# Kernel optimization log

Measured on AMD Instinct MI355X. Metric: run time of the kernel, lower is better.

Reference implementation:

```python
import jax, jax.numpy as jnp
import numpy as np

# graph structure constants (uniform graphs => simple coloring / masks all-true)
G, NV, EPG, LEPG = 128, 32, 64, 256          # graphs, nodes/graph, g-edges/graph, lg-edges/graph
NG, NLG, ELG, K = G * NV, G * EPG, G * LEPG, EPG  # K = n_colors = lg-nodes per graph
H, HF, T, L, NC, FIN, FE, NB = 32, 128, 8, 4, 12, 16, 16, 4  # hidden, hidden_final, towers, layers, classes, node feats, edge feats, basis

_FLOATS = ('x_g','edge_attr_g','x_lg','edge_attr_lg','W_enc','b_enc','W_msg','b_msg','W_init','b_init','np_l1_w','np_l1_b','np_l2_w','np_l2_b','np_lin_w','np_lin_b','fe_l1_w','fe_l1_b','fe_l2_w','fe_l2_b','fe_lin_w','fe_lin_b','gd_w','gd_b','ga_w','ga_b','ld_w','ld_b','la_w','la_b','u1_w','u1_b','u2_w','u2_b','u3_w','u3_b','en_w','en_b','li_w','li_b','lj_w','lj_b','bn_g','bn_b','ac_w','ac_b','fl_w','fl_b')

def _lin(x, w, b):
    return x @ w + b

def _glin(x, w, b):
    # grouped (tower) linear: w [T, c, c], block-diagonal over channel groups
    t, ci, co = w.shape
    y = jnp.einsum('...tc,tcd->...td', x.reshape(x.shape[:-1] + (t, ci)), w)
    return y.reshape(x.shape[:-1] + (t * co,)) + b

def setup_inputs():
    rng = np.random.default_rng(0)
    off_n = np.arange(G)[:, None] * NV
    ei_g = np.stack([(rng.integers(0, NV, (G, EPG)) + off_n).ravel(),
                     (rng.integers(0, NV, (G, EPG)) + off_n).ravel()])
    off_e = np.arange(G)[:, None] * EPG
    ei_lg = np.stack([(rng.integers(0, EPG, (G, LEPG)) + off_e).ravel(),
                      (rng.integers(0, EPG, (G, LEPG)) + off_e).ravel()])
    keys = iter(jax.random.split(jax.random.key(0), 64))
    def nrm(shape, fan):
        return (jax.random.normal(next(keys), shape, dtype=jnp.float32) / np.float32(np.sqrt(fan)))
    z = lambda *s: jnp.zeros(s, jnp.float32)
    inp = {
        'x_g': nrm((NG, FIN), 1.0),
        'edge_attr_g': nrm((NLG, FE), 1.0),
        'x_lg': nrm((NLG, NB), 1.0),
        'edge_attr_lg': nrm((ELG, NB), 1.0),
        'W_enc': nrm((FIN, H), FIN), 'b_enc': z(H),
        'W_msg': nrm((2 * H + FE + NB, HF), 2 * H + FE + NB), 'b_msg': z(HF),
        'W_init': nrm((HF + 1, H), HF + 1), 'b_init': z(H),
        'np_l1_w': nrm((HF + 1, HF), HF + 1), 'np_l1_b': z(HF),
        'np_l2_w': nrm((HF + 1, HF), HF + 1), 'np_l2_b': z(HF),
        'np_lin_w': nrm((HF, HF), HF), 'np_lin_b': z(HF),
        'fe_l1_w': nrm((H, HF), H), 'fe_l1_b': z(HF),
        'fe_l2_w': nrm((H, HF), H), 'fe_l2_b': z(HF),
        'fe_lin_w': nrm((HF, HF), HF), 'fe_lin_b': z(HF),
        'gd_w': nrm((NB, NB), NB), 'gd_b': z(NB),
        'ga_w': nrm((NB, NB), NB), 'ga_b': z(NB),
        'ld_w': nrm((L, NB, H), NB), 'ld_b': z(L, H),
        'la_w': nrm((L, NB, H), NB), 'la_b': z(L, H),
        'u1_w': nrm((L, T, H // T, H // T), H // T), 'u1_b': z(L, H),
        'u2_w': nrm((L, T, H // T, H // T), H // T), 'u2_b': z(L, H),
        'u3_w': nrm((L, T, H // T, H // T), H // T), 'u3_b': z(L, H),
        'en_w': nrm((L, H, H), H), 'en_b': z(L, H),
        'li_w': nrm((L, T, H // T, H // T), H // T), 'li_b': z(L, H),
        'lj_w': nrm((L, T, H // T, H // T), H // T), 'lj_b': z(L, H),
        'bn_g': jnp.ones((L, H), jnp.float32), 'bn_b': z(L, H),
        'ac_w': nrm((HF, HF), HF), 'ac_b': z(HF),
        'fl_w': nrm((HF, NC), HF), 'fl_b': z(NC),
        'edge_index_g': jnp.asarray(ei_g, dtype=jnp.int32),
        'edge_index_lg': jnp.asarray(ei_lg, dtype=jnp.int32),
        'batch_g': jnp.asarray(np.repeat(np.arange(G), NV), dtype=jnp.int32),
    }
    return inp

def _forward(fl, edge_index_g, edge_index_lg, batch_g):
    p = dict(zip(_FLOATS, fl))
    h = _lin(p['x_g'], p['W_enc'], p['b_enc'])                                 # [NG, H]
    s, d = edge_index_g[0], edge_index_g[1]
    hm = _lin(jnp.concatenate([h[s], h[d], p['edge_attr_g'], p['x_lg']], -1),
              p['W_msg'], p['b_msg'])                                          # [NLG, HF]
    batch_lg = batch_g[s]                                                      # graph id per lg node
    coloring = jnp.arange(NLG, dtype=jnp.int32) - batch_lg * EPG               # local color in [0, K)
    onehot = (coloring[:, None] == jnp.arange(K)).astype(hm.dtype)             # [NLG, K]
    # map_x_to_u: one-hot identity channel + features on own color row
    u = jnp.concatenate([onehot[:, :, None], onehot[:, :, None] * hm[:, None, :]], 2)  # [NLG, K, HF+1]
    edge_glob = _lin(p['edge_attr_lg'], p['ga_w'], p['ga_b'])                  # [ELG, NB]
    dist_glob = _lin(p['x_lg'], p['gd_w'], p['gd_b'])                          # [NLG, NB]
    ls, ld = edge_index_lg[0], edge_index_lg[1]
    indeg = jax.ops.segment_sum(jnp.ones((ELG,), hm.dtype), ld, num_segments=NLG)
    avg_e = (jax.ops.segment_sum(indeg, batch_lg, num_segments=G) / EPG)[batch_lg]  # avg edges/graph per node
    idx = jnp.arange(NLG)
    nb = jnp.asarray(EPG, hm.dtype)                                            # lg nodes per graph

    def extract(u, w1, b1, w2, b2, lw, lb):
        # GraphExtractor: UtoGlobal (mean-over-colors pool + diagonal pool) + residual relu lin
        mean = jax.ops.segment_sum(u.sum(1) / nb, batch_lg, num_segments=G) / nb
        diag = jax.ops.segment_sum(u[idx, coloring], batch_lg, num_segments=G) / nb
        out = _lin(mean, w1, b1) + _lin(diag, w2, b2)
        return out + jax.nn.relu(_lin(out, lw, lb))

    out = extract(u, p['np_l1_w'], p['np_l1_b'], p['np_l2_w'], p['np_l2_b'], p['np_lin_w'], p['np_lin_b'])
    u = _lin(u, p['W_init'], p['b_init'])                                      # [NLG, K, H]
    for i in range(L):
        if i > 0:  # batch norm (training-mode stats over nodes x colors)
            m = u.mean((0, 1)); v = u.var((0, 1))
            u = (u - m) * jax.lax.rsqrt(v + 1e-5) * p['bn_g'][i] + p['bn_b'][i]
        dist_loc = _lin(dist_glob, p['ld_w'][i], p['ld_b'][i])                 # [NLG, H]
        edge_loc = _lin(edge_glob, p['la_w'][i], p['la_b'][i])                 # [ELG, H]
        # SMPLayer: UtoU message net (entrywise + color-mean + diagonal terms, towered)
        um = (_glin(u, p['u1_w'][i], p['u1_b'][i])
              + _glin(u.sum(1) / nb, p['u2_w'][i], p['u2_b'][i])[:, None, :]
              + _glin(u[idx, coloring], p['u3_w'][i], p['u3_b'][i])[:, None, :])
        um = um * dist_loc[:, None, :]                                         # distance-basis filter
        ui = _glin(um, p['li_w'][i], p['li_b'][i])
        uj = _glin(um, p['lj_w'][i], p['lj_b'][i])
        ef = _lin(edge_loc, p['en_w'][i], p['en_b'][i])[:, None, :]
        msg = um[ls] + jax.nn.relu(ui[ld] + uj[ls] + ef)                       # [ELG, K, H]
        u = jax.ops.segment_sum(msg, ld, num_segments=NLG) / avg_e[:, None, None] + u
        out = out + extract(u, p['fe_l1_w'], p['fe_l1_b'], p['fe_l2_w'], p['fe_l2_b'], p['fe_lin_w'], p['fe_lin_b']) / L
    out = jax.nn.relu(_lin(out, p['ac_w'], p['ac_b'])) + out
    return _lin(out, p['fl_w'], p['fl_b'])                                     # [G, NC]

def reference(x_g, edge_attr_g, x_lg, edge_attr_lg, W_enc, b_enc, W_msg, b_msg, W_init, b_init, np_l1_w, np_l1_b, np_l2_w, np_l2_b, np_lin_w, np_lin_b, fe_l1_w, fe_l1_b, fe_l2_w, fe_l2_b, fe_lin_w, fe_lin_b, gd_w, gd_b, ga_w, ga_b, ld_w, ld_b, la_w, la_b, u1_w, u1_b, u2_w, u2_b, u3_w, u3_b, en_w, en_b, li_w, li_b, lj_w, lj_b, bn_g, bn_b, ac_w, ac_b, fl_w, fl_b, edge_index_g, edge_index_lg, batch_g):
    args = dict(locals())
    fl = tuple(args[n] for n in _FLOATS)
    return _forward(fl, edge_index_g, edge_index_lg, batch_g)
```

## Files before the change

kernel.cpp:

```cpp
#include <hip/hip_runtime.h>

#define G_    128
#define NV_   32
#define EPG_  64
#define LEPG_ 256
#define NG_   (G_*NV_)
#define NLG_  (G_*EPG_)
#define ELG_  (G_*LEPG_)
#define K_    64
#define H_    32
#define HF_   128
#define L_    4
#define NC_   12
#define FIN_  16
#define FE_   16
#define NB_   4
#define TILE_ (K_*H_)

__global__ void k_init(float* sc, float* sh, float* bn_acc) {
    int t = threadIdx.x;
    if (t < 32) { sc[t] = 1.0f; sh[t] = 0.0f; }
    if (t < 256) bn_acc[t] = 0.0f;
}

__global__ void k_enc(const float* __restrict__ xg, const float* __restrict__ W,
                      const float* __restrict__ b, float* __restrict__ h) {
    int gid = blockIdx.x * 256 + threadIdx.x;
    int n = gid >> 5, ch = gid & 31;
    float s = b[ch];
#pragma unroll
    for (int f = 0; f < FIN_; ++f) s += xg[n*FIN_ + f] * W[f*H_ + ch];
    h[gid] = s;
}

__global__ __launch_bounds__(128) void k_msg(
    const float* __restrict__ h, const float* __restrict__ eag,
    const float* __restrict__ xlg, const int* __restrict__ sidx,
    const int* __restrict__ didx, const float* __restrict__ W,
    const float* __restrict__ b, float* __restrict__ hm) {
    __shared__ float in[84];
    int i = blockIdx.x, t = threadIdx.x;
    int s = sidx[i], d = didx[i];
    if (t < 32)       in[t] = h[s*H_ + t];
    else if (t < 64)  in[t] = h[d*H_ + (t-32)];
    else if (t < 80)  in[t] = eag[i*FE_ + (t-64)];
    else if (t < 84)  in[t] = xlg[i*NB_ + (t-80)];
    __syncthreads();
    float o = b[t];
    for (int k = 0; k < 84; ++k) o += in[k] * W[k*HF_ + t];
    hm[i*HF_ + t] = o;
}

__global__ void k_glob(const float* __restrict__ ealg, const float* __restrict__ gaw,
                       const float* __restrict__ gab, const float* __restrict__ xlg,
                       const float* __restrict__ gdw, const float* __restrict__ gdb,
                       float* __restrict__ eglob, float* __restrict__ dglob) {
    int gid = blockIdx.x * 256 + threadIdx.x;
    if (gid < ELG_*4) {
        int e = gid >> 2, k = gid & 3;
        float s = gab[k];
#pragma unroll
        for (int j = 0; j < 4; ++j) s += ealg[e*4+j] * gaw[j*4+k];
        eglob[gid] = s;
    }
    int gid2 = gid - ELG_*4;
    if (gid2 >= 0 && gid2 < NLG_*4) {
        int n = gid2 >> 2, k = gid2 & 3;
        float s = gdb[k];
#pragma unroll
        for (int j = 0; j < 4; ++j) s += xlg[n*4+j] * gdw[j*4+k];
        dglob[gid2] = s;
    }
}

__global__ __launch_bounds__(128) void k_out0(
    const float* __restrict__ hm, const float* __restrict__ l1w,
    const float* __restrict__ l1b, const float* __restrict__ l2w,
    const float* __restrict__ l2b, const float* __restrict__ lnw,
    const float* __restrict__ lnb, float* __restrict__ out_acc) {
    __shared__ float mh[128], o1[128];
    int g = blockIdx.x, t = threadIdx.x;
    float s = 0.f;
    for (int k = 0; k < 64; ++k) s += hm[(g*64+k)*HF_ + t];
    mh[t] = s * (1.f/64.f);
    __syncthreads();
    float o = l1b[t] + l2b[t] + (l1w[t]*(1.f/64.f) + l2w[t]);
    for (int k = 0; k < 128; ++k)
        o += mh[k] * (l1w[(1+k)*HF_ + t]*(1.f/64.f) + l2w[(1+k)*HF_ + t]);
    o1[t] = o;
    __syncthreads();
    float r = lnb[t];
    for (int k = 0; k < 128; ++k) r += o1[k] * lnw[k*HF_ + t];
    out_acc[g*HF_ + t] = o + (r > 0.f ? r : 0.f);
}

__global__ __launch_bounds__(256) void k_u0(
    const float* __restrict__ hm, const float* __restrict__ Wi,
    const float* __restrict__ bi, float* __restrict__ u0,
    float* __restrict__ nst) {
    __shared__ float rv[32];
    int n = blockIdx.x, t = threadIdx.x, cn = n & 63;
    if (t < 32) {
        float s = Wi[t];
        for (int f = 0; f < HF_; ++f) s += hm[n*HF_ + f] * Wi[(1+f)*H_ + t];
        rv[t] = s;
    }
    __syncthreads();
#pragma unroll
    for (int k = 0; k < 8; ++k) {
        int idx = t + k*256;
        int ch = idx >> 6, c = idx & 63;
        u0[(size_t)n*TILE_ + idx] = bi[ch] + (c == cn ? rv[ch] : 0.f);
    }
    if (t < 32) {
        nst[n*96 + t]      = 64.f*bi[t] + rv[t];
        nst[n*96 + 32 + t] = bi[t] + rv[t];
    }
}

__global__ void k_dl(const float* __restrict__ dgl, const float* __restrict__ ldw,
                     const float* __restrict__ ldb, float* __restrict__ dlb) {
    int gid = blockIdx.x * 256 + threadIdx.x;
    int n = gid >> 5, ch = gid & 31;
    float s = ldb[ch];
#pragma unroll
    for (int j = 0; j < 4; ++j) s += dgl[n*4+j] * ldw[j*32 + ch];
    dlb[gid] = s;
}

__global__ __launch_bounds__(128) void k_ef(
    const float* __restrict__ egl, const float* __restrict__ law,
    const float* __restrict__ lab, const float* __restrict__ enw,
    const float* __restrict__ enb, float* __restrict__ efb) {
    __shared__ float el[128];
    int t = threadIdx.x;
    int eL = t >> 5, ch = t & 31;
    int e = blockIdx.x * 4 + eL;
    float s = lab[ch];
#pragma unroll
    for (int j = 0; j < 4; ++j) s += egl[e*4+j] * law[j*32 + ch];
    el[t] = s;
    __syncthreads();
    float o = enb[ch];
    for (int k = 0; k < 32; ++k) o += el[eL*32 + k] * enw[k*32 + ch];
    efb[e*32 + ch] = o;
}

__global__ __launch_bounds__(256) void k_gt(
    const float* __restrict__ nst, const float* __restrict__ sc,
    const float* __restrict__ sh, const float* __restrict__ u1w,
    const float* __restrict__ u2w, const float* __restrict__ u3w,
    const float* __restrict__ u1b, const float* __restrict__ u2b,
    const float* __restrict__ u3b, const float* __restrict__ dlb,
    float* __restrict__ gtdl) {
    int gid = blockIdx.x * 256 + threadIdx.x;
    int n = gid >> 5, ch = gid & 31;
    int chi = ch & 3, twb = ch & ~3;
    float gt = u1b[ch] + u2b[ch] + u3b[ch];
#pragma unroll
    for (int j = 0; j < 4; ++j) {
        int bj = twb + j;
        float scv = sc[bj], shv = sh[bj];
        float csF = scv*nst[n*96 + bj] + 64.f*shv;
        float dgF = scv*nst[n*96 + 32 + bj] + shv;
        gt += csF*(1.f/64.f)*u2w[bj*4 + chi] + dgF*u3w[bj*4 + chi]
            + shv*u1w[bj*4 + chi];
    }
    gtdl[gid] = gt * dlb[n*32 + ch];
}

__global__ __launch_bounds__(256) void k_layer(
    const float* __restrict__ u_in, float* __restrict__ u_out,
    const int* __restrict__ ls, const int* __restrict__ ld,
    const float* __restrict__ sc, const float* __restrict__ sh,
    const float* __restrict__ u1w,
    const float* __restrict__ liw, const float* __restrict__ lib,
    const float* __restrict__ ljw, const float* __restrict__ ljb,
    const float* __restrict__ dl, const float* __restrict__ gtdl,
    const float* __restrict__ ef, float* __restrict__ node_stats) {
    const int n = blockIdx.x;
    const int g = n >> 6, cn = n & 63;
    const int t = threadIdx.x;
    const int s = t >> 6;
    const int lane = t & 63;
    const int q = lane >> 3, chL = lane & 7;
    const int ch = s*8 + chL;
    const int chi = ch & 3, twb = ch & ~3;

    float w1m[4], wim[4], wjm[4];
#pragma unroll
    for (int m = 0; m < 4; ++m) {
        int jj = chi ^ m;
        w1m[m] = u1w[(twb + jj)*4 + chi] * sc[twb + jj];
        wim[m] = liw[(twb + jj)*4 + chi];
        wjm[m] = ljw[(twb + jj)*4 + chi];
    }
    const float scc = sc[ch], shc = sh[ch];
    const float bli = lib[ch], blj = ljb[ch];
    const float dlo = dl[(n<<5) + ch], gto = gtdl[(n<<5) + ch];

    const int eoff = (ch << 6) + (q << 3);

    float uo[8];
    {
        const float4* p4 = (const float4*)(u_in + ((size_t)n << 11) + eoff);
        float4 A = p4[0], B = p4[1];
        uo[0]=A.x; uo[1]=A.y; uo[2]=A.z; uo[3]=A.w;
        uo[4]=B.x; uo[5]=B.y; uo[6]=B.z; uo[7]=B.w;
    }

    float ui_[8];
#pragma unroll
    for (int j = 0; j < 8; ++j) {
        float v1 = __shfl_xor(uo[j], 1);
        float v2 = __shfl_xor(uo[j], 2);
        float v3 = __shfl_xor(uo[j], 3);
        float um = (uo[j]*w1m[0] + v1*w1m[1] + v2*w1m[2] + v3*w1m[3]) * dlo + gto;
        float m1 = __shfl_xor(um, 1);
        float m2 = __shfl_xor(um, 2);
        float m3 = __shfl_xor(um, 3);
        ui_[j] = bli + um*wim[0] + m1*wim[1] + m2*wim[2] + m3*wim[3];
    }

    float acc[8];
#pragma unroll
    for (int j = 0; j < 8; ++j) acc[j] = 0.f;

    const int ebase = g << 8;
    for (int r = 0; r < 4; ++r) {
        int d = ld[ebase + (r << 6) + lane];
        unsigned long long mask = __ballot(d == n);
        while (mask) {
            int b = __ffsll((unsigned long long)mask) - 1;
            mask &= mask - 1;
            int e = ebase + (r << 6) + b;
            int src = ls[e];
            const float4* p4 = (const float4*)(u_in + ((size_t)src << 11) + eoff);
            float4 A = p4[0], B = p4[1];
            float us[8] = {A.x,A.y,A.z,A.w,B.x,B.y,B.z,B.w};
            float dls = dl[(src<<5) + ch];
            float gts = gtdl[(src<<5) + ch];
            float efe = ef[(e<<5) + ch];
#pragma unroll
            for (int j = 0; j < 8; ++j) {
                float v1 = __shfl_xor(us[j], 1);
                float v2 = __shfl_xor(us[j], 2);
                float v3 = __shfl_xor(us[j], 3);
                float um = (us[j]*w1m[0] + v1*w1m[1] + v2*w1m[2] + v3*w1m[3]) * dls + gts;
                float m1 = __shfl_xor(um, 1);
                float m2 = __shfl_xor(um, 2);
                float m3 = __shfl_xor(um, 3);
                float uj = blj + um*wjm[0] + m1*wjm[1] + m2*wjm[2] + m3*wjm[3];
                float rr = ui_[j] + uj + efe;
                acc[j] += um + (rr > 0.f ? rr : 0.f);
            }
        }
    }

    float un[8], csum = 0.f, ssum = 0.f;
#pragma unroll
    for (int j = 0; j < 8; ++j) {
        un[j] = acc[j]*0.25f + (scc*uo[j] + shc);
        csum += un[j];
        ssum += un[j]*un[j];
    }
    {
        float4 A = make_float4(un[0],un[1],un[2],un[3]);
        float4 B = make_float4(un[4],un[5],un[6],un[7]);
        float4* p4 = (float4*)(u_out + ((size_t)n << 11) + eoff);
        p4[0] = A; p4[1] = B;
    }
    csum += __shfl_xor(csum, 8);  ssum += __shfl_xor(ssum, 8);
    csum += __shfl_xor(csum, 16); ssum += __shfl_xor(ssum, 16);
    csum += __shfl_xor(csum, 32); ssum += __shfl_xor(ssum, 32);
    if (q == 0) {
        node_stats[n*96 + ch]      = csum;
        node_stats[n*96 + 64 + ch] = ssum;
    }
    if (q == (cn >> 3)) {
        float dv;
        switch (cn & 7) {
            case 0: dv = un[0]; break; case 1: dv = un[1]; break;
            case 2: dv = un[2]; break; case 3: dv = un[3]; break;
            case 4: dv = un[4]; break; case 5: dv = un[5]; break;
            case 6: dv = un[6]; break; default: dv = un[7]; break;
        }
        node_stats[n*96 + 32 + ch] = dv;
    }
}

__global__ __launch_bounds__(256) void k_extract(
    const float* __restrict__ nst,
    const float* __restrict__ l1w, const float* __restrict__ l1b,
    const float* __restrict__ l2w, const float* __restrict__ l2b,
    const float* __restrict__ lnw, const float* __restrict__ lnb,
    float* __restrict__ out_acc, float* __restrict__ bn_acc, float scale) {
    __shared__ float red[192];
    __shared__ float S[32], D[32], o1[128];
    int g = blockIdx.x, t = threadIdx.x;
    if (t < 192) {
        int half = t / 96, slot = t % 96;
        float s = 0.f;
        const float* p = nst + (size_t)(g*64 + half*32)*96 + slot;
        for (int k = 0; k < 32; ++k) s += p[k*96];
        red[t] = s;
    }
    __syncthreads();
    if (t < 96) {
        float s = red[t] + red[96 + t];
        if (t < 32)      { S[t] = s; atomicAdd(&bn_acc[t], s); }
        else if (t < 64) { D[t-32] = s; }
        else             { atomicAdd(&bn_acc[t-32], s); }
    }
    __syncthreads();
    float o = 0.f;
    if (t < 128) {
        o = l1b[t] + l2b[t];
        for (int k = 0; k < 32; ++k)
            o += (S[k]*(1.f/4096.f))*l1w[k*HF_ + t] + (D[k]*(1.f/64.f))*l2w[k*HF_ + t];
        o1[t] = o;
    }
    __syncthreads();
    if (t < 128) {
        float r = lnb[t];
        for (int k = 0; k < 128; ++k) r += o1[k] * lnw[k*HF_ + t];
        out_acc[g*HF_ + t] += (o + (r > 0.f ? r : 0.f)) * scale;
    }
}

__global__ void k_bnfold(const float* __restrict__ bn_acc,
                         const float* __restrict__ bng, const float* __restrict__ bnb,
                         float* __restrict__ sc, float* __restrict__ sh) {
    int ch = threadIdx.x;
    float m = bn_acc[ch] * (1.f/524288.f);
    float v = bn_acc[32+ch] * (1.f/524288.f) - m*m;
    float s = bng[ch] * rsqrtf(v + 1e-5f);
    sc[ch] = s;
    sh[ch] = bnb[ch] - m*s;
}

__global__ __launch_bounds__(128) void k_final(
    const float* __restrict__ out_acc, const float* __restrict__ acw,
    const float* __restrict__ acb, const float* __restrict__ flw,
    const float* __restrict__ flb, float* __restrict__ out) {
    __shared__ float t1[128];
    int g = blockIdx.x, t = threadIdx.x;
    float o = out_acc[g*HF_ + t];
    float r = acb[t];
    for (int k = 0; k < 128; ++k) r += out_acc[g*HF_ + k] * acw[k*HF_ + t];
    t1[t] = o + (r > 0.f ? r : 0.f);
    __syncthreads();
    if (t < NC_) {
        float s = flb[t];
        for (int k = 0; k < 128; ++k) s += t1[k] * flw[k*NC_ + t];
        out[g*NC_ + t] = s;
    }
}

extern "C" void kernel_launch(void* const* d_in, const int* in_sizes, int n_in,
                              void* d_out, int out_size, void* d_ws, size_t ws_size,
                              hipStream_t stream) {
    const float* x_g      = (const float*)d_in[0];
    const float* eag      = (const float*)d_in[1];
    const float* x_lg     = (const float*)d_in[2];
    const float* ealg     = (const float*)d_in[3];
    const float* W_enc    = (const float*)d_in[4];
    const float* b_enc    = (const float*)d_in[5];
    const float* W_msg    = (const float*)d_in[6];
    const float* b_msg    = (const float*)d_in[7];
    const float* W_init   = (const float*)d_in[8];
    const float* b_init   = (const float*)d_in[9];
    const float* np_l1_w  = (const float*)d_in[10];
    const float* np_l1_b  = (const float*)d_in[11];
    const float* np_l2_w  = (const float*)d_in[12];
    const float* np_l2_b  = (const float*)d_in[13];
    const float* np_lin_w = (const float*)d_in[14];
    const float* np_lin_b = (const float*)d_in[15];
    const float* fe_l1_w  = (const float*)d_in[16];
    const float* fe_l1_b  = (const float*)d_in[17];
    const float* fe_l2_w  = (const float*)d_in[18];
    const float* fe_l2_b  = (const float*)d_in[19];
    const float* fe_lin_w = (const float*)d_in[20];
    const float* fe_lin_b = (const float*)d_in[21];
    const float* gd_w     = (const float*)d_in[22];
    const float* gd_b     = (const float*)d_in[23];
    const float* ga_w     = (const float*)d_in[24];
    const float* ga_b     = (const float*)d_in[25];
    const float* ld_w     = (const float*)d_in[26];
    const float* ld_b     = (const float*)d_in[27];
    const float* la_w     = (const float*)d_in[28];
    const float* la_b     = (const float*)d_in[29];
    const float* u1_w     = (const float*)d_in[30];
    const float* u1_b     = (const float*)d_in[31];
    const float* u2_w     = (const float*)d_in[32];
    const float* u2_b     = (const float*)d_in[33];
    const float* u3_w     = (const float*)d_in[34];
    const float* u3_b     = (const float*)d_in[35];
    const float* en_w     = (const float*)d_in[36];
    const float* en_b     = (const float*)d_in[37];
    const float* li_w     = (const float*)d_in[38];
    const float* li_b     = (const float*)d_in[39];
    const float* lj_w     = (const float*)d_in[40];
    const float* lj_b     = (const float*)d_in[41];
    const float* bn_g     = (const float*)d_in[42];
    const float* bn_b     = (const float*)d_in[43];
    const float* ac_w     = (const float*)d_in[44];
    const float* ac_b     = (const float*)d_in[45];
    const float* fl_w     = (const float*)d_in[46];
    const float* fl_b     = (const float*)d_in[47];
    const int*   ei_g     = (const int*)d_in[48];
    const int*   ei_lg    = (const int*)d_in[49];

    const int* s_g  = ei_g;
    const int* d_g  = ei_g + NLG_;
    const int* ls   = ei_lg;
    const int* ldst = ei_lg + ELG_;

    float* ws = (float*)d_ws;
    size_t o = 0;
    float* ub0  = ws + o; o += (size_t)NLG_ * TILE_;
    float* ub1  = ws + o; o += (size_t)NLG_ * TILE_;
    float* hm   = ws + o; o += (size_t)NLG_ * HF_;
    float* hbuf = ws + o; o += (size_t)NG_ * H_;
    float* dgl  = ws + o; o += (size_t)NLG_ * NB_;
    float* egl  = ws + o; o += (size_t)ELG_ * NB_;
    float* nst  = ws + o; o += (size_t)NLG_ * 96;
    float* oac  = ws + o; o += (size_t)G_ * HF_;
    float* bna  = ws + o; o += 256;
    float* scb  = ws + o; o += 128;
    float* shb  = ws + o; o += 128;
    float* dlb  = ws + o; o += (size_t)NLG_ * 32;
    float* gtb  = ws + o; o += (size_t)NLG_ * 32;
    float* efb  = ws + o; o += (size_t)ELG_ * 32;

    k_init<<<1, 256, 0, stream>>>(scb, shb, bna);
    k_enc<<<(NG_*H_)/256, 256, 0, stream>>>(x_g, W_enc, b_enc, hbuf);
    k_msg<<<NLG_, 128, 0, stream>>>(hbuf, eag, x_lg, s_g, d_g, W_msg, b_msg, hm);
    k_glob<<<(ELG_*4 + NLG_*4 + 255)/256, 256, 0, stream>>>(
        ealg, ga_w, ga_b, x_lg, gd_w, gd_b, egl, dgl);
    k_out0<<<G_, 128, 0, stream>>>(hm, np_l1_w, np_l1_b, np_l2_w, np_l2_b,
                                   np_lin_w, np_lin_b, oac);
    k_u0<<<NLG_, 256, 0, stream>>>(hm, W_init, b_init, ub0, nst);

    float* ubufs[2] = {ub0, ub1};
    for (int i = 0; i < L_; ++i) {
        const float* ui = ubufs[i & 1];
        float* uo = ubufs[(i + 1) & 1];
        if (i > 0)
            k_bnfold<<<1, 32, 0, stream>>>(bna + (i-1)*64, bn_g + i*32,
                                           bn_b + i*32, scb + i*32, shb + i*32);
        k_dl<<<(NLG_*32)/256, 256, 0, stream>>>(dgl, ld_w + i*128, ld_b + i*32, dlb);
        k_ef<<<ELG_/4, 128, 0, stream>>>(egl, la_w + i*128, la_b + i*32,
                                         en_w + i*1024, en_b + i*32, efb);
        k_gt<<<(NLG_*32)/256, 256, 0, stream>>>(
            nst, scb + i*32, shb + i*32,
            u1_w + i*128, u2_w + i*128, u3_w + i*128,
            u1_b + i*32, u2_b + i*32, u3_b + i*32, dlb, gtb);
        k_layer<<<NLG_, 256, 0, stream>>>(
            ui, uo, ls, ldst,
            scb + i*32, shb + i*32,
            u1_w + i*128,
            li_w + i*128, li_b + i*32,
            lj_w + i*128, lj_b + i*32,
            dlb, gtb, efb, nst);
        k_extract<<<G_, 256, 0, stream>>>(
            nst, fe_l1_w, fe_l1_b, fe_l2_w, fe_l2_b, fe_lin_w, fe_lin_b,
            oac, bna + i*64, 1.0f / (float)L_);
    }
    k_final<<<G_, 128, 0, stream>>>(oac, ac_w, ac_b, fl_w, fl_b, (float*)d_out);
}
```

Measured before the change: 698.8 us.

## Fuse per-layer prep kernels into layer kernel, precompute edge masks, prefetch edges

Merges the encoder and global projection kernels into one launch. The per-layer dl/ef projections are hoisted into a single launch that covers all layers, and the gt and BN-fold computations are folded into k_layer. Per-node incoming-edge ballot masks are computed once in k_u0 instead of rebuilding the ballot in every layer. k_layer also software-prefetches the next edge's source tile, and blocks are swizzled so graphs interleave. This cuts launch count and redundant work at the cost of more workspace, double-buffered node stats, and higher register pressure in k_layer.

```diff
diff --git a/kernel.cpp b/kernel.cpp
--- a/kernel.cpp
+++ b/kernel.cpp
@@ -17,20 +17,45 @@
 #define NB_   4
 #define TILE_ (K_*H_)
 
-__global__ void k_init(float* sc, float* sh, float* bn_acc) {
-    int t = threadIdx.x;
-    if (t < 32) { sc[t] = 1.0f; sh[t] = 0.0f; }
-    if (t < 256) bn_acc[t] = 0.0f;
-}
-
-__global__ void k_enc(const float* __restrict__ xg, const float* __restrict__ W,
-                      const float* __restrict__ b, float* __restrict__ h) {
-    int gid = blockIdx.x * 256 + threadIdx.x;
-    int n = gid >> 5, ch = gid & 31;
-    float s = b[ch];
-#pragma unroll
-    for (int f = 0; f < FIN_; ++f) s += xg[n*FIN_ + f] * W[f*H_ + ch];
-    h[gid] = s;
+__device__ __forceinline__ void swz_node(int bid, int& g, int& v, int& n) {
+    g = ((bid >> 9) << 3) | (bid & 7);
+    v = (bid >> 3) & 63;
+    n = (g << 6) | v;
+}
+
+__global__ __launch_bounds__(256) void k_pre(
+    const float* __restrict__ xg, const float* __restrict__ Wenc,
+    const float* __restrict__ benc,
+    const float* __restrict__ ealg, const float* __restrict__ gaw,
+    const float* __restrict__ gab,
+    const float* __restrict__ xlg, const float* __restrict__ gdw,
+    const float* __restrict__ gdb,
+    float* __restrict__ h, float* __restrict__ eglob, float* __restrict__ dglob)
+{
+    int bid = blockIdx.x, t = threadIdx.x;
+    if (bid < 512) {
+        int gid = bid*256 + t; int nn = gid>>5, ch = gid&31;
+        float s = benc[ch];
+#pragma unroll
+        for (int f = 0; f < FIN_; ++f) s += xg[nn*FIN_+f]*Wenc[f*H_+ch];
+        h[gid] = s;
+    } else {
+        int gid = (bid-512)*256 + t;
+        if (gid < ELG_*4) {
+            int e = gid>>2, k = gid&3;
+            float s = gab[k];
+#pragma unroll
+            for (int j = 0; j < 4; ++j) s += ealg[e*4+j]*gaw[j*4+k];
+            eglob[gid] = s;
+        } else {
+            int gid2 = gid - ELG_*4;
+            int nn = gid2>>2, k = gid2&3;
+            float s = gdb[k];
+#pragma unroll
+            for (int j = 0; j < 4; ++j) s += xlg[nn*4+j]*gdw[j*4+k];
+            dglob[gid2] = s;
+        }
+    }
 }
 
 __global__ __launch_bounds__(128) void k_msg(
@@ -51,28 +76,6 @@
     hm[i*HF_ + t] = o;
 }
 
-__global__ void k_glob(const float* __restrict__ ealg, const float* __restrict__ gaw,
-                       const float* __restrict__ gab, const float* __restrict__ xlg,
-                       const float* __restrict__ gdw, const float* __restrict__ gdb,
-                       float* __restrict__ eglob, float* __restrict__ dglob) {
-    int gid = blockIdx.x * 256 + threadIdx.x;
-    if (gid < ELG_*4) {
-        int e = gid >> 2, k = gid & 3;
-        float s = gab[k];
-#pragma unroll
-        for (int j = 0; j < 4; ++j) s += ealg[e*4+j] * gaw[j*4+k];
-        eglob[gid] = s;
-    }
-    int gid2 = gid - ELG_*4;
-    if (gid2 >= 0 && gid2 < NLG_*4) {
-        int n = gid2 >> 2, k = gid2 & 3;
-        float s = gdb[k];
-#pragma unroll
-        for (int j = 0; j < 4; ++j) s += xlg[n*4+j] * gdw[j*4+k];
-        dglob[gid2] = s;
-    }
-}
-
 __global__ __launch_bounds__(128) void k_out0(
     const float* __restrict__ hm, const float* __restrict__ l1w,
     const float* __restrict__ l1b, const float* __restrict__ l2w,
@@ -96,15 +99,28 @@
 
 __global__ __launch_bounds__(256) void k_u0(
     const float* __restrict__ hm, const float* __restrict__ Wi,
-    const float* __restrict__ bi, float* __restrict__ u0,
-    float* __restrict__ nst) {
+    const float* __restrict__ bi, const int* __restrict__ ldst,
+    float* __restrict__ u0, float* __restrict__ nst,
+    unsigned long long* __restrict__ mskb, float* __restrict__ bna) {
     __shared__ float rv[32];
-    int n = blockIdx.x, t = threadIdx.x, cn = n & 63;
+    int bid = blockIdx.x, t = threadIdx.x;
+    int g, v, n; swz_node(bid, g, v, n);
+    int cn = v;
+    if (bid == 0) bna[t] = 0.f;
     if (t < 32) {
         float s = Wi[t];
         for (int f = 0; f < HF_; ++f) s += hm[n*HF_ + f] * Wi[(1+f)*H_ + t];
         rv[t] = s;
     }
+    if (t < 64) {
+        int ebase = g << 8;
+#pragma unroll
+        for (int r = 0; r < 4; ++r) {
+            int d = ldst[ebase + (r<<6) + t];
+            unsigned long long mk = __ballot(d == n);
+            if (t == 0) mskb[n*4 + r] = mk;
+        }
+    }
     __syncthreads();
 #pragma unroll
     for (int k = 0; k < 8; ++k) {
@@ -118,143 +134,180 @@
     }
 }
 
-__global__ void k_dl(const float* __restrict__ dgl, const float* __restrict__ ldw,
-                     const float* __restrict__ ldb, float* __restrict__ dlb) {
-    int gid = blockIdx.x * 256 + threadIdx.x;
-    int n = gid >> 5, ch = gid & 31;
-    float s = ldb[ch];
-#pragma unroll
-    for (int j = 0; j < 4; ++j) s += dgl[n*4+j] * ldw[j*32 + ch];
-    dlb[gid] = s;
-}
-
-__global__ __launch_bounds__(128) void k_ef(
-    const float* __restrict__ egl, const float* __restrict__ law,
-    const float* __restrict__ lab, const float* __restrict__ enw,
-    const float* __restrict__ enb, float* __restrict__ efb) {
-    __shared__ float el[128];
-    int t = threadIdx.x;
-    int eL = t >> 5, ch = t & 31;
-    int e = blockIdx.x * 4 + eL;
-    float s = lab[ch];
-#pragma unroll
-    for (int j = 0; j < 4; ++j) s += egl[e*4+j] * law[j*32 + ch];
-    el[t] = s;
-    __syncthreads();
-    float o = enb[ch];
-    for (int k = 0; k < 32; ++k) o += el[eL*32 + k] * enw[k*32 + ch];
-    efb[e*32 + ch] = o;
-}
-
-__global__ __launch_bounds__(256) void k_gt(
-    const float* __restrict__ nst, const float* __restrict__ sc,
-    const float* __restrict__ sh, const float* __restrict__ u1w,
-    const float* __restrict__ u2w, const float* __restrict__ u3w,
-    const float* __restrict__ u1b, const float* __restrict__ u2b,
-    const float* __restrict__ u3b, const float* __restrict__ dlb,
-    float* __restrict__ gtdl) {
-    int gid = blockIdx.x * 256 + threadIdx.x;
-    int n = gid >> 5, ch = gid & 31;
-    int chi = ch & 3, twb = ch & ~3;
-    float gt = u1b[ch] + u2b[ch] + u3b[ch];
-#pragma unroll
-    for (int j = 0; j < 4; ++j) {
-        int bj = twb + j;
-        float scv = sc[bj], shv = sh[bj];
-        float csF = scv*nst[n*96 + bj] + 64.f*shv;
-        float dgF = scv*nst[n*96 + 32 + bj] + shv;
-        gt += csF*(1.f/64.f)*u2w[bj*4 + chi] + dgF*u3w[bj*4 + chi]
-            + shv*u1w[bj*4 + chi];
-    }
-    gtdl[gid] = gt * dlb[n*32 + ch];
+__global__ __launch_bounds__(256) void k_dlef(
+    const float* __restrict__ dgl, const float* __restrict__ egl,
+    const float* __restrict__ ldw, const float* __restrict__ ldb,
+    const float* __restrict__ law, const float* __restrict__ lab,
+    const float* __restrict__ enw, const float* __restrict__ enb,
+    float* __restrict__ dlb, float* __restrict__ efb) {
+    int bid = blockIdx.x, t = threadIdx.x;
+    if (bid < 4096) {
+        int gid = bid*256 + t;
+        int l = gid >> 18, rem = gid & ((1<<18)-1);
+        int n = rem >> 5, ch = rem & 31;
+        float s = ldb[l*32 + ch];
+#pragma unroll
+        for (int j = 0; j < 4; ++j) s += dgl[n*4+j] * ldw[l*128 + j*32 + ch];
+        dlb[gid] = s;
+    } else {
+        __shared__ float el[8][32];
+        int p = (bid - 4096)*8 + (t >> 5);
+        int ch = t & 31;
+        int l = p >> 15, e = p & 32767;
+        float s = lab[l*32 + ch];
+#pragma unroll
+        for (int j = 0; j < 4; ++j) s += egl[e*4+j] * law[l*128 + j*32 + ch];
+        el[t>>5][ch] = s;
+        __syncthreads();
+        float o = enb[l*32 + ch];
+        for (int k = 0; k < 32; ++k) o += el[t>>5][k] * enw[l*1024 + k*32 + ch];
+        efb[(size_t)l*ELG_*32 + e*32 + ch] = o;
+    }
 }
 
 __global__ __launch_bounds__(256) void k_layer(
     const float* __restrict__ u_in, float* __restrict__ u_out,
-    const int* __restrict__ ls, const int* __restrict__ ld,
-    const float* __restrict__ sc, const float* __restrict__ sh,
-    const float* __restrict__ u1w,
+    const int* __restrict__ ls, const unsigned long long* __restrict__ mskb,
+    const float* __restrict__ bnaP, const float* __restrict__ bngL,
+    const float* __restrict__ bnbL, int layer,
+    const float* __restrict__ u1w, const float* __restrict__ u2w,
+    const float* __restrict__ u3w, const float* __restrict__ u1b,
+    const float* __restrict__ u2b, const float* __restrict__ u3b,
     const float* __restrict__ liw, const float* __restrict__ lib,
     const float* __restrict__ ljw, const float* __restrict__ ljb,
-    const float* __restrict__ dl, const float* __restrict__ gtdl,
-    const float* __restrict__ ef, float* __restrict__ node_stats) {
-    const int n = blockIdx.x;
-    const int g = n >> 6, cn = n & 63;
+    const float* __restrict__ dlp, const float* __restrict__ efp,
+    const float* __restrict__ nin, float* __restrict__ nout)
+{
+    const int bid = blockIdx.x;
+    int g, v, n; swz_node(bid, g, v, n);
     const int t = threadIdx.x;
     const int s = t >> 6;
     const int lane = t & 63;
     const int q = lane >> 3, chL = lane & 7;
     const int ch = s*8 + chL;
     const int chi = ch & 3, twb = ch & ~3;
-
-    float w1m[4], wim[4], wjm[4];
-#pragma unroll
-    for (int m = 0; m < 4; ++m) {
-        int jj = chi ^ m;
-        w1m[m] = u1w[(twb + jj)*4 + chi] * sc[twb + jj];
-        wim[m] = liw[(twb + jj)*4 + chi];
-        wjm[m] = ljw[(twb + jj)*4 + chi];
-    }
-    const float scc = sc[ch], shc = sh[ch];
-    const float bli = lib[ch], blj = ljb[ch];
-    const float dlo = dl[(n<<5) + ch], gto = gtdl[(n<<5) + ch];
-
+    const int cn = v;
+    const int ebase = g << 8;
     const int eoff = (ch << 6) + (q << 3);
+
+    unsigned long long m0 = mskb[n*4+0], m1 = mskb[n*4+1],
+                       m2 = mskb[n*4+2], m3 = mskb[n*4+3];
 
     float uo[8];
     {
         const float4* p4 = (const float4*)(u_in + ((size_t)n << 11) + eoff);
         float4 A = p4[0], B = p4[1];
-        uo[0]=A.x; uo[1]=A.y; uo[2]=A.z; uo[3]=A.w;
-        uo[4]=B.x; uo[5]=B.y; uo[6]=B.z; uo[7]=B.w;
-    }
+        uo[0]=A.x;uo[1]=A.y;uo[2]=A.z;uo[3]=A.w;uo[4]=B.x;uo[5]=B.y;uo[6]=B.z;uo[7]=B.w;
+    }
+    const float dlo = dlp[(n<<5)+ch];
+    float ocs[4], odg[4];
+    {
+        const float* snp = nin + n*96;
+#pragma unroll
+        for (int mm = 0; mm < 4; ++mm) {
+            int bj = twb + (chi^mm); ocs[mm] = snp[bj]; odg[mm] = snp[32+bj];
+        }
+    }
+
+    float w1m[4], wim[4], wjm[4], aj[4], bjv[4];
+    float scc = 1.f, shc = 0.f;
+    float C = u1b[ch] + u2b[ch] + u3b[ch];
+#pragma unroll
+    for (int mm = 0; mm < 4; ++mm) {
+        int jj = chi ^ mm; int bj = twb + jj;
+        float s_ = 1.f, m_ = 0.f, sh_ = 0.f;
+        if (layer != 0) {
+            m_ = bnaP[bj] * (1.f/524288.f);
+            float v_ = bnaP[32+bj] * (1.f/524288.f) - m_*m_;
+            s_ = bngL[bj] * rsqrtf(v_ + 1e-5f);
+            sh_ = bnbL[bj] - m_*s_;
+        }
+        float w1v = u1w[bj*4+chi], w2v = u2w[bj*4+chi], w3v = u3w[bj*4+chi];
+        w1m[mm] = w1v * s_;
+        wim[mm] = liw[bj*4+chi];
+        wjm[mm] = ljw[bj*4+chi];
+        aj[mm]  = s_ * w2v * (1.f/64.f);
+        bjv[mm] = s_ * w3v;
+        C += sh_ * (w1v + w2v + w3v);
+        if (mm == 0) { scc = s_; shc = sh_; }
+    }
+    const float bli = lib[ch], blj = ljb[ch];
+
+    int rr_ = 0; unsigned long long mc = m0;
+    auto nexte = [&]() -> int {
+        for (;;) {
+            if (mc) { int b = __ffsll(mc) - 1; mc &= mc - 1; return ebase + (rr_<<6) + b; }
+            ++rr_;
+            if (rr_ == 1) mc = m1; else if (rr_ == 2) mc = m2;
+            else if (rr_ == 3) mc = m3; else return -1;
+        }
+    };
+
+    int eA = nexte(); int eAc = (eA >= 0) ? eA : ebase; int sA = ls[eAc];
+    float4 A0, A1; float dlA, efA; float acs[4], adg[4];
+    {
+        const float4* p4 = (const float4*)(u_in + ((size_t)sA << 11) + eoff);
+        A0 = p4[0]; A1 = p4[1];
+        dlA = dlp[(sA<<5)+ch]; efA = efp[(eAc<<5)+ch];
+        const float* sp = nin + sA*96;
+#pragma unroll
+        for (int mm = 0; mm < 4; ++mm) {
+            int bj = twb + (chi^mm); acs[mm] = sp[bj]; adg[mm] = sp[32+bj];
+        }
+    }
+    int eB = (eA >= 0) ? nexte() : -1; int eBc = (eB >= 0) ? eB : ebase; int sB = ls[eBc];
 
     float ui_[8];
-#pragma unroll
-    for (int j = 0; j < 8; ++j) {
-        float v1 = __shfl_xor(uo[j], 1);
-        float v2 = __shfl_xor(uo[j], 2);
-        float v3 = __shfl_xor(uo[j], 3);
-        float um = (uo[j]*w1m[0] + v1*w1m[1] + v2*w1m[2] + v3*w1m[3]) * dlo + gto;
-        float m1 = __shfl_xor(um, 1);
-        float m2 = __shfl_xor(um, 2);
-        float m3 = __shfl_xor(um, 3);
-        ui_[j] = bli + um*wim[0] + m1*wim[1] + m2*wim[2] + m3*wim[3];
+    {
+        float gto = C + aj[0]*ocs[0]+aj[1]*ocs[1]+aj[2]*ocs[2]+aj[3]*ocs[3]
+                      + bjv[0]*odg[0]+bjv[1]*odg[1]+bjv[2]*odg[2]+bjv[3]*odg[3];
+        float gtdlo = gto * dlo;
+#pragma unroll
+        for (int j = 0; j < 8; ++j) {
+            float v1=__shfl_xor(uo[j],1), v2=__shfl_xor(uo[j],2), v3=__shfl_xor(uo[j],3);
+            float um = (uo[j]*w1m[0]+v1*w1m[1]+v2*w1m[2]+v3*w1m[3])*dlo + gtdlo;
+            float n1=__shfl_xor(um,1), n2=__shfl_xor(um,2), n3=__shfl_xor(um,3);
+            ui_[j] = bli + um*wim[0]+n1*wim[1]+n2*wim[2]+n3*wim[3];
+        }
     }
 
     float acc[8];
 #pragma unroll
     for (int j = 0; j < 8; ++j) acc[j] = 0.f;
 
-    const int ebase = g << 8;
-    for (int r = 0; r < 4; ++r) {
-        int d = ld[ebase + (r << 6) + lane];
-        unsigned long long mask = __ballot(d == n);
-        while (mask) {
-            int b = __ffsll((unsigned long long)mask) - 1;
-            mask &= mask - 1;
-            int e = ebase + (r << 6) + b;
-            int src = ls[e];
-            const float4* p4 = (const float4*)(u_in + ((size_t)src << 11) + eoff);
-            float4 A = p4[0], B = p4[1];
-            float us[8] = {A.x,A.y,A.z,A.w,B.x,B.y,B.z,B.w};
-            float dls = dl[(src<<5) + ch];
-            float gts = gtdl[(src<<5) + ch];
-            float efe = ef[(e<<5) + ch];
+    while (eA >= 0) {
+        int eC = (eB >= 0) ? nexte() : -1; int eCc = (eC >= 0) ? eC : ebase;
+        int sC = ls[eCc];
+        float4 B0, B1; float dlB, efB; float bcs[4], bdg[4];
+        {
+            const float4* p4 = (const float4*)(u_in + ((size_t)sB << 11) + eoff);
+            B0 = p4[0]; B1 = p4[1];
+            dlB = dlp[(sB<<5)+ch]; efB = efp[(eBc<<5)+ch];
+            const float* sp = nin + sB*96;
+#pragma unroll
+            for (int mm = 0; mm < 4; ++mm) {
+                int bj = twb + (chi^mm); bcs[mm] = sp[bj]; bdg[mm] = sp[32+bj];
+            }
+        }
+        {
+            float gts = C + aj[0]*acs[0]+aj[1]*acs[1]+aj[2]*acs[2]+aj[3]*acs[3]
+                          + bjv[0]*adg[0]+bjv[1]*adg[1]+bjv[2]*adg[2]+bjv[3]*adg[3];
+            float gtdl = gts * dlA;
+            float us[8] = {A0.x,A0.y,A0.z,A0.w,A1.x,A1.y,A1.z,A1.w};
 #pragma unroll
             for (int j = 0; j < 8; ++j) {
-                float v1 = __shfl_xor(us[j], 1);
-                float v2 = __shfl_xor(us[j], 2);
-                float v3 = __shfl_xor(us[j], 3);
-                float um = (us[j]*w1m[0] + v1*w1m[1] + v2*w1m[2] + v3*w1m[3]) * dls + gts;
-                float m1 = __shfl_xor(um, 1);
-                float m2 = __shfl_xor(um, 2);
-                float m3 = __shfl_xor(um, 3);
-                float uj = blj + um*wjm[0] + m1*wjm[1] + m2*wjm[2] + m3*wjm[3];
-                float rr = ui_[j] + uj + efe;
-                acc[j] += um + (rr > 0.f ? rr : 0.f);
+                float v1=__shfl_xor(us[j],1), v2=__shfl_xor(us[j],2), v3=__shfl_xor(us[j],3);
+                float um = (us[j]*w1m[0]+v1*w1m[1]+v2*w1m[2]+v3*w1m[3])*dlA + gtdl;
+                float n1=__shfl_xor(um,1), n2=__shfl_xor(um,2), n3=__shfl_xor(um,3);
+                float uj = blj + um*wjm[0]+n1*wjm[1]+n2*wjm[2]+n3*wjm[3];
+                float rr2 = ui_[j] + uj + efA;
+                acc[j] += um + (rr2 > 0.f ? rr2 : 0.f);
             }
         }
+        eA = eB; sA = sB; A0 = B0; A1 = B1; dlA = dlB; efA = efB;
+#pragma unroll
+        for (int mm = 0; mm < 4; ++mm) { acs[mm] = bcs[mm]; adg[mm] = bdg[mm]; }
+        eB = eC; eBc = eCc; sB = sC;
     }
 
     float un[8], csum = 0.f, ssum = 0.f;
@@ -274,8 +327,8 @@
     csum += __shfl_xor(csum, 16); ssum += __shfl_xor(ssum, 16);
     csum += __shfl_xor(csum, 32); ssum += __shfl_xor(ssum, 32);
     if (q == 0) {
-        node_stats[n*96 + ch]      = csum;
-        node_stats[n*96 + 64 + ch] = ssum;
+        nout[n*96 + ch]      = csum;
+        nout[n*96 + 64 + ch] = ssum;
     }
     if (q == (cn >> 3)) {
         float dv;
@@ -285,7 +338,7 @@
             case 4: dv = un[4]; break; case 5: dv = un[5]; break;
             case 6: dv = un[6]; break; default: dv = un[7]; break;
         }
-        node_stats[n*96 + 32 + ch] = dv;
+        nout[n*96 + 32 + ch] = dv;
     }
 }
 
@@ -326,17 +379,6 @@
         for (int k = 0; k < 128; ++k) r += o1[k] * lnw[k*HF_ + t];
         out_acc[g*HF_ + t] += (o + (r > 0.f ? r : 0.f)) * scale;
     }
-}
-
-__global__ void k_bnfold(const float* __restrict__ bn_acc,
-                         const float* __restrict__ bng, const float* __restrict__ bnb,
-                         float* __restrict__ sc, float* __restrict__ sh) {
-    int ch = threadIdx.x;
-    float m = bn_acc[ch] * (1.f/524288.f);
-    float v = bn_acc[32+ch] * (1.f/524288.f) - m*m;
-    float s = bng[ch] * rsqrtf(v + 1e-5f);
-    sc[ch] = s;
-    sh[ch] = bnb[ch] - m*s;
 }
 
 __global__ __launch_bounds__(128) void k_final(
@@ -418,53 +460,47 @@
 
     float* ws = (float*)d_ws;
     size_t o = 0;
+    unsigned long long* mskb = (unsigned long long*)ws; o += NLG_ * 4 * 2;
     float* ub0  = ws + o; o += (size_t)NLG_ * TILE_;
     float* ub1  = ws + o; o += (size_t)NLG_ * TILE_;
     float* hm   = ws + o; o += (size_t)NLG_ * HF_;
     float* hbuf = ws + o; o += (size_t)NG_ * H_;
     float* dgl  = ws + o; o += (size_t)NLG_ * NB_;
     float* egl  = ws + o; o += (size_t)ELG_ * NB_;
-    float* nst  = ws + o; o += (size_t)NLG_ * 96;
+    float* nstA = ws + o; o += (size_t)NLG_ * 96;
+    float* nstB = ws + o; o += (size_t)NLG_ * 96;
     float* oac  = ws + o; o += (size_t)G_ * HF_;
     float* bna  = ws + o; o += 256;
-    float* scb  = ws + o; o += 128;
-    float* shb  = ws + o; o += 128;
-    float* dlb  = ws + o; o += (size_t)NLG_ * 32;
-    float* gtb  = ws + o; o += (size_t)NLG_ * 32;
-    float* efb  = ws + o; o += (size_t)ELG_ * 32;
-
-    k_init<<<1, 256, 0, stream>>>(scb, shb, bna);
-    k_enc<<<(NG_*H_)/256, 256, 0, stream>>>(x_g, W_enc, b_enc, hbuf);
+    float* dlb  = ws + o; o += (size_t)L_ * NLG_ * 32;
+    float* efb  = ws + o; o += (size_t)L_ * ELG_ * 32;
+
+    k_pre<<<1152, 256, 0, stream>>>(x_g, W_enc, b_enc, ealg, ga_w, ga_b,
+                                    x_lg, gd_w, gd_b, hbuf, egl, dgl);
     k_msg<<<NLG_, 128, 0, stream>>>(hbuf, eag, x_lg, s_g, d_g, W_msg, b_msg, hm);
-    k_glob<<<(ELG_*4 + NLG_*4 + 255)/256, 256, 0, stream>>>(
-        ealg, ga_w, ga_b, x_lg, gd_w, gd_b, egl, dgl);
+    k_dlef<<<4096 + 16384, 256, 0, stream>>>(dgl, egl, ld_w, ld_b, la_w, la_b,
+                                             en_w, en_b, dlb, efb);
     k_out0<<<G_, 128, 0, stream>>>(hm, np_l1_w, np_l1_b, np_l2_w, np_l2_b,
                                    np_lin_w, np_lin_b, oac);
-    k_u0<<<NLG_, 256, 0, stream>>>(hm, W_init, b_init, ub0, nst);
+    k_u0<<<NLG_, 256, 0, stream>>>(hm, W_init, b_init, ldst, ub0, nstA, mskb, bna);
 
     float* ubufs[2] = {ub0, ub1};
+    float* nbufs[2] = {nstA, nstB};
     for (int i = 0; i < L_; ++i) {
         const float* ui = ubufs[i & 1];
         float* uo = ubufs[(i + 1) & 1];
-        if (i > 0)
-            k_bnfold<<<1, 32, 0, stream>>>(bna + (i-1)*64, bn_g + i*32,
-                                           bn_b + i*32, scb + i*32, shb + i*32);
-        k_dl<<<(NLG_*32)/256, 256, 0, stream>>>(dgl, ld_w + i*128, ld_b + i*32, dlb);
-        k_ef<<<ELG_/4, 128, 0, stream>>>(egl, la_w + i*128, la_b + i*32,
-                                         en_w + i*1024, en_b + i*32, efb);
-        k_gt<<<(NLG_*32)/256, 256, 0, stream>>>(
-            nst, scb + i*32, shb + i*32,
+        const float* ni = nbufs[i & 1];
+        float* no = nbufs[(i + 1) & 1];
+        k_layer<<<NLG_, 256, 0, stream>>>(
+            ui, uo, ls, mskb,
+            bna + (i > 0 ? (i-1)*64 : 0), bn_g + i*32, bn_b + i*32, i,
             u1_w + i*128, u2_w + i*128, u3_w + i*128,
-            u1_b + i*32, u2_b + i*32, u3_b + i*32, dlb, gtb);
-        k_layer<<<NLG_, 256, 0, stream>>>(
-            ui, uo, ls, ldst,
-            scb + i*32, shb + i*32,
-            u1_w + i*128,
+            u1_b + i*32, u2_b + i*32, u3_b + i*32,
             li_w + i*128, li_b + i*32,
             lj_w + i*128, lj_b + i*32,
-            dlb, gtb, efb, nst);
+            dlb + (size_t)i*NLG_*32, efb + (size_t)i*ELG_*32,
+            ni, no);
         k_extract<<<G_, 256, 0, stream>>>(
-            nst, fe_l1_w, fe_l1_b, fe_l2_w, fe_l2_b, fe_lin_w, fe_lin_b,
+            no, fe_l1_w, fe_l1_b, fe_l2_w, fe_l2_b, fe_lin_w, fe_lin_b,
             oac, bna + i*64, 1.0f / (float)L_);
     }
     k_final<<<G_, 128, 0, stream>>>(oac, ac_w, ac_b, fl_w, fl_b, (float*)d_out);
```

Result: slower. 720.1 us (+3.0%).
